# Kernel optimization log

Measured on AMD Instinct MI355X. Metric: run time of the kernel, lower is better.

The kernel has to match this reference:

```python
import jax, jax.numpy as jnp
import numpy as np


def setup_inputs() -> dict:
    key = jax.random.key(0)
    k1, k2, k3, k4, k5 = jax.random.split(key, 5)
    B, S, ENC, DEC = 32, 2048, 1024, 512
    hidden = jax.random.normal(k1, (B, DEC), dtype=jnp.float32)
    encoder_outputs = jax.random.normal(k2, (B, S, ENC), dtype=jnp.float32)
    W = jax.random.normal(k3, (DEC, ENC + DEC), dtype=jnp.float32) * (1.0 / np.sqrt(ENC + DEC))
    b = jax.random.normal(k4, (DEC,), dtype=jnp.float32) * 0.01
    v = jax.random.uniform(k5, (DEC,), dtype=jnp.float32)  # torch.rand init
    return {"hidden": hidden, "encoder_outputs": encoder_outputs, "W": W, "b": b, "v": v}


def reference(hidden, encoder_outputs, W, b, v):
    # hidden: [B, D_dec], encoder_outputs: [B, S, D_enc]
    # Concat order in original: (hidden, encoder_outputs) -> split W accordingly.
    D_dec = hidden.shape[-1]
    Wh = W[:, :D_dec]   # [D_dec, D_dec] acts on hidden
    We = W[:, D_dec:]   # [D_dec, D_enc] acts on encoder_outputs
    # energy: tanh(Linear(cat(hidden_repeated, enc))) == tanh(h@Wh^T + enc@We^T + b)
    h_proj = jnp.einsum('bd,ed->be', hidden, Wh)                 # [B, D_dec]
    e_proj = jnp.einsum('bse,de->bsd', encoder_outputs, We)      # [B, S, D_dec]
    energy = jnp.tanh(e_proj + h_proj[:, None, :] + b)           # [B, S, D_dec]
    # scores: v . energy per (b, s); softmax over src_len
    scores = jnp.einsum('d,bsd->bs', v, energy)                  # [B, S]
    attn = jax.nn.softmax(scores, axis=-1)
    return attn[:, None, :]                                       # [B, 1, S]
```

## Files before the change

kernel.cpp:

```cpp
#include <hip/hip_runtime.h>
#include <hip/hip_bf16.h>


typedef __attribute__((ext_vector_type(8))) short bf16x8;
typedef __attribute__((ext_vector_type(4))) float f32x4;

__device__ __forceinline__ ushort f2bf(float x) {
    __hip_bfloat16 h = __float2bfloat16(x);
    return *reinterpret_cast<ushort*>(&h);
}

__device__ __forceinline__ bf16x8 pack8(float4 a, float4 b) {
    bf16x8 o;
    o[0] = (short)f2bf(a.x); o[1] = (short)f2bf(a.y);
    o[2] = (short)f2bf(a.z); o[3] = (short)f2bf(a.w);
    o[4] = (short)f2bf(b.x); o[5] = (short)f2bf(b.y);
    o[6] = (short)f2bf(b.z); o[7] = (short)f2bf(b.w);
    return o;
}

#define WS_WBF   0
#define WS_HB    (1u << 20)
#define WS_SCORE ((1u << 20) + (64u << 10))

__global__ void prep_kernel(const float* __restrict__ W,
                            const float* __restrict__ hidden,
                            const float* __restrict__ bias,
                            ushort* __restrict__ Wbf,
                            float* __restrict__ hb,
                            float* __restrict__ score) {
    const int bid = blockIdx.x, tid = threadIdx.x;
    if (bid < 512) {
        int idx = bid * 256 + tid;
        int d  = idx >> 8;
        int e4 = (idx & 255) * 4;
        float4 f = *(const float4*)(W + (size_t)d * 1536 + 512 + e4);
        ushort4 u;
        u.x = f2bf(f.x); u.y = f2bf(f.y); u.z = f2bf(f.z); u.w = f2bf(f.w);
        *(ushort4*)(Wbf + (size_t)d * 1024 + e4) = u;
    } else if (bid < 576) {
        int idx = (bid - 512) * 256 + tid;
        int b = idx >> 9, d = idx & 511;
        const float4* hp = (const float4*)(hidden + b * 512);
        const float4* wp = (const float4*)(W + (size_t)d * 1536);
        float acc = 0.f;
#pragma unroll 8
        for (int j = 0; j < 128; ++j) {
            float4 h = hp[j], w = wp[j];
            acc += h.x * w.x + h.y * w.y + h.z * w.z + h.w * w.w;
        }
        hb[idx] = acc + bias[d];
    } else {
        int idx = (bid - 576) * 256 + tid;
        float4 z = {0.f, 0.f, 0.f, 0.f};
        *(float4*)(score + (size_t)idx * 4) = z;
    }
}

__launch_bounds__(256, 3)
__global__ void eproj_scores(const float* __restrict__ enc,
                             const ushort* __restrict__ Wbf,
                             const float* __restrict__ hb,
                             const float* __restrict__ v,
                             float* __restrict__ scores) {
    __shared__ alignas(16) ushort Abuf[4][2048];

    const int tid  = threadIdx.x;
    const int lane = tid & 63, w = tid >> 6;
    const int q = lane >> 4, ln = lane & 15;
    const int  swz  = (blockIdx.x & 7) * 256 + (blockIdx.x >> 3);
    const int  nblk = swz & 1;
    const long m0   = (long)(swz >> 1) * 64;
    const int  bidx = (int)(m0 >> 11);
    const int  n0   = nblk * 256 + w * 64;

    f32x4 acc[4][4];
#pragma unroll
    for (int mt = 0; mt < 4; ++mt)
#pragma unroll
        for (int nt = 0; nt < 4; ++nt)
            acc[mt][nt] = (f32x4){0.f, 0.f, 0.f, 0.f};

    const ushort* bptr[4];
#pragma unroll
    for (int nt = 0; nt < 4; ++nt)
        bptr[nt] = Wbf + (size_t)(n0 + nt * 16 + ln) * 1024 + q * 8;

    const int sr = tid >> 2, sq = tid & 3;
    const float* aptr = enc + (m0 + sr) * 1024 + sq * 8;
    const int awoff = sr * 32 + ((sq ^ (sr & 3)) << 3);

    int rdoff[4];
#pragma unroll
    for (int mt = 0; mt < 4; ++mt) {
        int rA = mt * 16 + ln;
        rdoff[mt] = rA * 32 + ((q ^ (rA & 3)) << 3);
    }

    float4 ar[2][2];
    ar[0][0] = *(const float4*)(aptr);
    ar[0][1] = *(const float4*)(aptr + 4);
    ar[1][0] = *(const float4*)(aptr + 32);
    ar[1][1] = *(const float4*)(aptr + 36);

    bf16x8 bfr[2][4];
#pragma unroll
    for (int nt = 0; nt < 4; ++nt)
        bfr[0][nt] = *(const bf16x8*)(bptr[nt]);

    *(bf16x8*)(&Abuf[0][awoff]) = pack8(ar[0][0], ar[0][1]);
    ar[0][0] = *(const float4*)(aptr + 64);
    ar[0][1] = *(const float4*)(aptr + 68);

    for (int g = 0; g < 8; ++g) {
#pragma unroll
        for (int j = 0; j < 4; ++j) {
            const int kt = g * 4 + j;
            const int p  = (j + 1) & 1;
            if (kt + 1 < 32) {
                *(bf16x8*)(&Abuf[(j + 1) & 3][awoff]) = pack8(ar[p][0], ar[p][1]);
                if (kt + 3 < 32) {
                    ar[p][0] = *(const float4*)(aptr + (kt + 3) * 32);
                    ar[p][1] = *(const float4*)(aptr + (kt + 3) * 32 + 4);
                }
                asm volatile("s_waitcnt lgkmcnt(0)" ::: "memory");
            }
            __builtin_amdgcn_s_barrier();
            asm volatile("" ::: "memory");

            if (kt + 1 < 32) {
#pragma unroll
                for (int nt = 0; nt < 4; ++nt)
                    bfr[p][nt] = *(const bf16x8*)(bptr[nt] + (size_t)(kt + 1) * 32);
            }
#pragma unroll
            for (int mt = 0; mt < 4; ++mt) {
                bf16x8 af = *(const bf16x8*)(&Abuf[j][rdoff[mt]]);
#pragma unroll
                for (int nt = 0; nt < 4; ++nt)
                    acc[mt][nt] = __builtin_amdgcn_mfma_f32_16x16x32_bf16(
                        af, bfr[j & 1][nt], acc[mt][nt], 0, 0, 0);
            }
        }
    }

    float partial[4][4];
#pragma unroll
    for (int mt = 0; mt < 4; ++mt)
#pragma unroll
        for (int r = 0; r < 4; ++r) partial[mt][r] = 0.f;

#pragma unroll
    for (int nt = 0; nt < 4; ++nt) {
        int d = n0 + nt * 16 + ln;
        float hbv = hb[bidx * 512 + d];
        float vv  = v[d];
#pragma unroll
        for (int mt = 0; mt < 4; ++mt)
#pragma unroll
            for (int r = 0; r < 4; ++r) {
                float x = acc[mt][nt][r] + hbv;
                float e = __expf(2.f * x);
                partial[mt][r] += vv * (1.f - 2.f / (e + 1.f));
            }
    }
#pragma unroll
    for (int mt = 0; mt < 4; ++mt)
#pragma unroll
        for (int r = 0; r < 4; ++r) {
            float s = partial[mt][r];
            s += __shfl_xor(s, 1);
            s += __shfl_xor(s, 2);
            s += __shfl_xor(s, 4);
            s += __shfl_xor(s, 8);
            partial[mt][r] = s;
        }

    __syncthreads();
    float* spart = (float*)Abuf;
    if (ln == 0) {
#pragma unroll
        for (int mt = 0; mt < 4; ++mt)
#pragma unroll
            for (int r = 0; r < 4; ++r)
                spart[w * 64 + mt * 16 + q * 4 + r] = partial[mt][r];
    }
    __syncthreads();
    if (tid < 64)
        atomicAdd(&scores[m0 + tid],
                  spart[tid] + spart[64 + tid] + spart[128 + tid] + spart[192 + tid]);
}

__global__ void softmax_kernel(const float* __restrict__ scores, float* __restrict__ out) {
    int b = blockIdx.x;
    const float* sc = scores + b * 2048;
    __shared__ float wred[4], wsum[4];

    float lmax = -1e30f;
    for (int i = threadIdx.x; i < 2048; i += 256) lmax = fmaxf(lmax, sc[i]);
#pragma unroll
    for (int m = 1; m < 64; m <<= 1) lmax = fmaxf(lmax, __shfl_xor(lmax, m));
    if ((threadIdx.x & 63) == 0) wred[threadIdx.x >> 6] = lmax;
    __syncthreads();
    float gmax = fmaxf(fmaxf(wred[0], wred[1]), fmaxf(wred[2], wred[3]));

    float lsum = 0.f;
    for (int i = threadIdx.x; i < 2048; i += 256) lsum += __expf(sc[i] - gmax);
#pragma unroll
    for (int m = 1; m < 64; m <<= 1) lsum += __shfl_xor(lsum, m);
    if ((threadIdx.x & 63) == 0) wsum[threadIdx.x >> 6] = lsum;
    __syncthreads();
    float inv = 1.f / (wsum[0] + wsum[1] + wsum[2] + wsum[3]);

    for (int i = threadIdx.x; i < 2048; i += 256)
        out[b * 2048 + i] = __expf(sc[i] - gmax) * inv;
}

extern "C" void kernel_launch(void* const* d_in, const int* in_sizes, int n_in,
                              void* d_out, int out_size, void* d_ws, size_t ws_size,
                              hipStream_t stream) {
    const float* hidden = (const float*)d_in[0];
    const float* enc    = (const float*)d_in[1];
    const float* W      = (const float*)d_in[2];
    const float* bias   = (const float*)d_in[3];
    const float* v      = (const float*)d_in[4];
    float* out = (float*)d_out;

    char* ws = (char*)d_ws;
    ushort* Wbf   = (ushort*)(ws + WS_WBF);
    float*  hb    = (float*)(ws + WS_HB);
    float*  score = (float*)(ws + WS_SCORE);

    hipLaunchKernelGGL(prep_kernel,  dim3(640),  dim3(256), 0, stream,
                       W, hidden, bias, Wbf, hb, score);
    hipLaunchKernelGGL(eproj_scores, dim3(2048), dim3(256), 0, stream,
                       enc, Wbf, hb, v, score);
    hipLaunchKernelGGL(softmax_kernel, dim3(32), dim3(256), 0, stream, score, out);
}
```

Measured before the change: 513.7 us.

## Use 512-thread blocks covering full N so each encoder tile is loaded once

The GEMM block grows from 256 to 512 threads (8 waves), each block covering all 512 output columns for a 64-row tile. Previously the block split N in two, so each encoder row tile was read and converted twice. Because one block now produces a whole score row, the zero-init pass and the atomicAdd are replaced by a direct store. The staging load per thread halves to one float4, and the 64-bit LDS writes may bring bank-conflict or occupancy changes.

```diff
diff --git a/kernel.cpp b/kernel.cpp
--- a/kernel.cpp
+++ b/kernel.cpp
@@ -10,12 +10,9 @@
     return *reinterpret_cast<ushort*>(&h);
 }
 
-__device__ __forceinline__ bf16x8 pack8(float4 a, float4 b) {
-    bf16x8 o;
-    o[0] = (short)f2bf(a.x); o[1] = (short)f2bf(a.y);
-    o[2] = (short)f2bf(a.z); o[3] = (short)f2bf(a.w);
-    o[4] = (short)f2bf(b.x); o[5] = (short)f2bf(b.y);
-    o[6] = (short)f2bf(b.z); o[7] = (short)f2bf(b.w);
+__device__ __forceinline__ ushort4 pack4(float4 a) {
+    ushort4 o;
+    o.x = f2bf(a.x); o.y = f2bf(a.y); o.z = f2bf(a.z); o.w = f2bf(a.w);
     return o;
 }
 
@@ -27,8 +24,7 @@
                             const float* __restrict__ hidden,
                             const float* __restrict__ bias,
                             ushort* __restrict__ Wbf,
-                            float* __restrict__ hb,
-                            float* __restrict__ score) {
+                            float* __restrict__ hb) {
     const int bid = blockIdx.x, tid = threadIdx.x;
     if (bid < 512) {
         int idx = bid * 256 + tid;
@@ -38,7 +34,7 @@
         ushort4 u;
         u.x = f2bf(f.x); u.y = f2bf(f.y); u.z = f2bf(f.z); u.w = f2bf(f.w);
         *(ushort4*)(Wbf + (size_t)d * 1024 + e4) = u;
-    } else if (bid < 576) {
+    } else {
         int idx = (bid - 512) * 256 + tid;
         int b = idx >> 9, d = idx & 511;
         const float4* hp = (const float4*)(hidden + b * 512);
@@ -50,14 +46,10 @@
             acc += h.x * w.x + h.y * w.y + h.z * w.z + h.w * w.w;
         }
         hb[idx] = acc + bias[d];
-    } else {
-        int idx = (bid - 576) * 256 + tid;
-        float4 z = {0.f, 0.f, 0.f, 0.f};
-        *(float4*)(score + (size_t)idx * 4) = z;
-    }
-}
-
-__launch_bounds__(256, 3)
+    }
+}
+
+__launch_bounds__(512, 2)
 __global__ void eproj_scores(const float* __restrict__ enc,
                              const ushort* __restrict__ Wbf,
                              const float* __restrict__ hb,
@@ -68,11 +60,9 @@
     const int tid  = threadIdx.x;
     const int lane = tid & 63, w = tid >> 6;
     const int q = lane >> 4, ln = lane & 15;
-    const int  swz  = (blockIdx.x & 7) * 256 + (blockIdx.x >> 3);
-    const int  nblk = swz & 1;
-    const long m0   = (long)(swz >> 1) * 64;
+    const long m0   = (long)blockIdx.x * 64;
     const int  bidx = (int)(m0 >> 11);
-    const int  n0   = nblk * 256 + w * 64;
+    const int  n0   = w * 64;
 
     f32x4 acc[4][4];
 #pragma unroll
@@ -86,9 +76,9 @@
     for (int nt = 0; nt < 4; ++nt)
         bptr[nt] = Wbf + (size_t)(n0 + nt * 16 + ln) * 1024 + q * 8;
 
-    const int sr = tid >> 2, sq = tid & 3;
-    const float* aptr = enc + (m0 + sr) * 1024 + sq * 8;
-    const int awoff = sr * 32 + ((sq ^ (sr & 3)) << 3);
+    const int sr = tid >> 3, sq = tid & 7;
+    const float* aptr = enc + (m0 + sr) * 1024 + sq * 4;
+    const int awoff = sr * 32 + (((sq >> 1) ^ (sr & 3)) << 3) + (sq & 1) * 4;
 
     int rdoff[4];
 #pragma unroll
@@ -97,20 +87,17 @@
         rdoff[mt] = rA * 32 + ((q ^ (rA & 3)) << 3);
     }
 
-    float4 ar[2][2];
-    ar[0][0] = *(const float4*)(aptr);
-    ar[0][1] = *(const float4*)(aptr + 4);
-    ar[1][0] = *(const float4*)(aptr + 32);
-    ar[1][1] = *(const float4*)(aptr + 36);
+    float4 ar[2];
+    ar[0] = *(const float4*)(aptr);
+    ar[1] = *(const float4*)(aptr + 32);
 
     bf16x8 bfr[2][4];
 #pragma unroll
     for (int nt = 0; nt < 4; ++nt)
         bfr[0][nt] = *(const bf16x8*)(bptr[nt]);
 
-    *(bf16x8*)(&Abuf[0][awoff]) = pack8(ar[0][0], ar[0][1]);
-    ar[0][0] = *(const float4*)(aptr + 64);
-    ar[0][1] = *(const float4*)(aptr + 68);
+    *(ushort4*)(&Abuf[0][awoff]) = pack4(ar[0]);
+    ar[0] = *(const float4*)(aptr + 64);
 
     for (int g = 0; g < 8; ++g) {
 #pragma unroll
@@ -118,11 +105,9 @@
             const int kt = g * 4 + j;
             const int p  = (j + 1) & 1;
             if (kt + 1 < 32) {
-                *(bf16x8*)(&Abuf[(j + 1) & 3][awoff]) = pack8(ar[p][0], ar[p][1]);
-                if (kt + 3 < 32) {
-                    ar[p][0] = *(const float4*)(aptr + (kt + 3) * 32);
-                    ar[p][1] = *(const float4*)(aptr + (kt + 3) * 32 + 4);
-                }
+                *(ushort4*)(&Abuf[(j + 1) & 3][awoff]) = pack4(ar[p]);
+                if (kt + 3 < 32)
+                    ar[p] = *(const float4*)(aptr + (kt + 3) * 32);
                 asm volatile("s_waitcnt lgkmcnt(0)" ::: "memory");
             }
             __builtin_amdgcn_s_barrier();
@@ -186,9 +171,12 @@
                 spart[w * 64 + mt * 16 + q * 4 + r] = partial[mt][r];
     }
     __syncthreads();
-    if (tid < 64)
-        atomicAdd(&scores[m0 + tid],
-                  spart[tid] + spart[64 + tid] + spart[128 + tid] + spart[192 + tid]);
+    if (tid < 64) {
+        float s = 0.f;
+#pragma unroll
+        for (int ww = 0; ww < 8; ++ww) s += spart[ww * 64 + tid];
+        scores[m0 + tid] = s;
+    }
 }
 
 __global__ void softmax_kernel(const float* __restrict__ scores, float* __restrict__ out) {
@@ -231,9 +219,9 @@
     float*  hb    = (float*)(ws + WS_HB);
     float*  score = (float*)(ws + WS_SCORE);
 
-    hipLaunchKernelGGL(prep_kernel,  dim3(640),  dim3(256), 0, stream,
-                       W, hidden, bias, Wbf, hb, score);
-    hipLaunchKernelGGL(eproj_scores, dim3(2048), dim3(256), 0, stream,
+    hipLaunchKernelGGL(prep_kernel,  dim3(576),  dim3(256), 0, stream,
+                       W, hidden, bias, Wbf, hb);
+    hipLaunchKernelGGL(eproj_scores, dim3(1024), dim3(512), 0, stream,
                        enc, Wbf, hb, v, score);
     hipLaunchKernelGGL(softmax_kernel, dim3(32), dim3(256), 0, stream, score, out);
 }
```

Result: no change. 513.5 us (-0.0%).
